# Kernel tuning notes

Measured on AMD Instinct MI355X. Metric: run time of the kernel, lower is better.

The kernel has to match this reference:

```python
import jax, jax.numpy as jnp
import numpy as np

N_SLOTS = 524288
DIM_MEM = 128
DIM_IN = 1024
SHIFT_RADIUS = 3
EPS = 1e-8  # torch cosine_similarity eps


def setup_inputs() -> dict:
    key = jax.random.key(0)
    k1, k2, k3, k4, k5 = jax.random.split(key, 5)
    n_factors = DIM_MEM + 1 + 1 + (2 * SHIFT_RADIUS + 1) + 1  # 138
    return {
        "input_from_controller": jax.random.normal(k1, (DIM_IN,), dtype=jnp.float32),
        "previous_weighting": jax.random.uniform(k2, (N_SLOTS,), dtype=jnp.float32),
        "memory": jax.random.normal(k3, (N_SLOTS, DIM_MEM), dtype=jnp.float32),
        "W_wf": jax.random.normal(k4, (DIM_IN, n_factors), dtype=jnp.float32) * 0.02,
        "b_wf": jax.random.normal(k5, (n_factors,), dtype=jnp.float32) * 0.02,
    }


def _get_weighting(input_from_controller, previous_weighting, memory, W_wf, b_wf):
    factors = input_from_controller @ W_wf + b_wf  # [138]
    M = DIM_MEM
    key_v = factors[:M]                       # [M]
    key_s = factors[M]                        # scalar (beta)
    gate = jax.nn.softmax(factors[M + 1:M + 2])      # size-1 softmax -> 1.0 (faithful)
    shift_w = jax.nn.softmax(factors[M + 2:M + 2 + 2 * SHIFT_RADIUS + 1])  # [2r+1]
    sharpening = jax.nn.relu(factors[-1]) + 1.0

    # content addressing: cosine similarity of each memory row with key_v
    mem_norm = jnp.maximum(jnp.linalg.norm(memory, axis=1), EPS)  # [N]
    key_norm = jnp.maximum(jnp.linalg.norm(key_v), EPS)
    content_w = (memory @ key_v) / (mem_norm * key_norm)          # [N]
    content_w = jax.nn.softmax(key_s * content_w)

    gated_w = content_w * gate[0] + (1.0 - gate[0]) * previous_weighting

    # circular convolution: shifted[i] = sum_j gated[(i - r + j) % N] * shift_w[j]
    shifted_w = jnp.zeros_like(gated_w)
    for j in range(2 * SHIFT_RADIUS + 1):  # small fixed tap count (7)
        shifted_w = shifted_w + shift_w[j] * jnp.roll(gated_w, SHIFT_RADIUS - j)

    pw = shifted_w ** sharpening
    return pw / pw.sum()


def reference(input_from_controller, previous_weighting, memory, W_wf, b_wf):
    w = _get_weighting(input_from_controller, previous_weighting, memory, W_wf, b_wf)
    read_vector = w @ memory  # read head forward
    return read_vector
```

## Files before the change

kernel.cpp:

```cpp
#include <hip/hip_runtime.h>
#include <math.h>

#define N_SLOTS 524288
#define DIM_MEM 128
#define DIM_IN 1024
#define NFACT 138
#define EPSF 1e-8f

#define RPB 256
#define CHUNK 64
#define NCH (RPB / CHUNK)
#define FB (N_SLOTS / RPB)

#define WS_NEED ((size_t)4096 + (size_t)(DIM_MEM + 1) * FB * 4)

__global__ __launch_bounds__(256) void k_factors(const float* __restrict__ x,
                                                 const float* __restrict__ W,
                                                 const float* __restrict__ b,
                                                 float* __restrict__ factors) {
    __shared__ float wred[4];
    const int j = blockIdx.x;
    const int t = threadIdx.x;
    float acc = 0.f;
    #pragma unroll
    for (int i = t; i < DIM_IN; i += 256)
        acc = fmaf(x[i], W[(size_t)i * NFACT + j], acc);
    #pragma unroll
    for (int off = 32; off; off >>= 1) acc += __shfl_xor(acc, off, 64);
    if ((t & 63) == 0) wred[t >> 6] = acc;
    __syncthreads();
    if (t == 0)
        factors[j] = wred[0] + wred[1] + wred[2] + wred[3] + b[j];
}

__global__ __launch_bounds__(256) void k_fused(const float* __restrict__ mem,
                                               const float* __restrict__ f,
                                               float* __restrict__ sc) {
    __shared__ float d_sh[12];
    __shared__ float e_sh[CHUNK + 8];
    __shared__ float w_sh[CHUNK];
    __shared__ float colpart[8][DIM_MEM];
    __shared__ float psum[8];

    const int tid  = threadIdx.x;
    const int lane = tid & 31;
    const int hw   = tid >> 5;

    if (tid < 64) {
        float fl = f[tid], fh = f[tid + 64];
        float v = fl * fl + fh * fh;
        #pragma unroll
        for (int off = 32; off; off >>= 1) v += __shfl_xor(v, off, 64);
        if (tid == 0) {
            float key_norm = fmaxf(sqrtf(v), EPSF);
            d_sh[0] = f[128] / key_norm;
            float m = f[130];
            #pragma unroll
            for (int q = 1; q < 7; ++q) m = fmaxf(m, f[130 + q]);
            float e[7], s = 0.f;
            #pragma unroll
            for (int q = 0; q < 7; ++q) { e[q] = __expf(f[130 + q] - m); s += e[q]; }
            #pragma unroll
            for (int q = 0; q < 7; ++q) d_sh[1 + q] = e[q] / s;
            d_sh[8] = fmaxf(f[137], 0.f) + 1.f;
        }
    }
    __syncthreads();

    const float4* __restrict__ mem4 = (const float4*)mem;
    const float4 k4 = ((const float4*)f)[lane];
    const float d0 = d_sh[0];
    const float sharp = d_sh[8];
    float sw[7];
    #pragma unroll
    for (int d = 0; d < 7; ++d) sw[d] = d_sh[1 + d];

    float4 acc = make_float4(0.f, 0.f, 0.f, 0.f);
    float wsum = 0.f;
    const int base = blockIdx.x * RPB;

    float4 row[2][8];
    #pragma unroll
    for (int j = 0; j < 8; ++j)
        row[0][j] = mem4[(size_t)(base + hw * 8 + j) * 32 + lane];

    #pragma unroll
    for (int c = 0; c < NCH; ++c) {
        const int cur = c & 1;
        const int nxt = cur ^ 1;
        const int r0 = base + c * CHUNK;

        #pragma unroll
        for (int j = 0; j < 8; ++j) {
            float4 m = row[cur][j];
            float dp = m.x * k4.x + m.y * k4.y + m.z * k4.z + m.w * k4.w;
            float np = m.x * m.x + m.y * m.y + m.z * m.z + m.w * m.w;
            #pragma unroll
            for (int off = 16; off; off >>= 1) {
                dp += __shfl_xor(dp, off, 32);
                np += __shfl_xor(np, off, 32);
            }
            if (lane == 0)
                e_sh[3 + hw * 8 + j] = __expf(d0 * dp / fmaxf(sqrtf(np), EPSF));
        }
        if (hw < 6) {
            int hr = (hw < 3) ? (r0 - 3 + hw) : (r0 + CHUNK + (hw - 3));
            hr &= (N_SLOTS - 1);
            const int p = (hw < 3) ? hw : (CHUNK + hw);
            float4 m = mem4[(size_t)hr * 32 + lane];
            float dp = m.x * k4.x + m.y * k4.y + m.z * k4.z + m.w * k4.w;
            float np = m.x * m.x + m.y * m.y + m.z * m.z + m.w * m.w;
            #pragma unroll
            for (int off = 16; off; off >>= 1) {
                dp += __shfl_xor(dp, off, 32);
                np += __shfl_xor(np, off, 32);
            }
            if (lane == 0)
                e_sh[p] = __expf(d0 * dp / fmaxf(sqrtf(np), EPSF));
        }
        if (c + 1 < NCH) {
            const int nb = r0 + CHUNK + hw * 8;
            #pragma unroll
            for (int j = 0; j < 8; ++j)
                row[nxt][j] = mem4[(size_t)(nb + j) * 32 + lane];
        }
        __syncthreads();

        if (tid < CHUNK) {
            float t = 0.f;
            #pragma unroll
            for (int d = 0; d < 7; ++d) t = fmaf(sw[d], e_sh[tid + d], t);
            w_sh[tid] = __expf(sharp * __logf(t));
        }
        __syncthreads();

        #pragma unroll
        for (int j = 0; j < 8; ++j) {
            float w = w_sh[hw * 8 + j];
            acc.x = fmaf(w, row[cur][j].x, acc.x);
            acc.y = fmaf(w, row[cur][j].y, acc.y);
            acc.z = fmaf(w, row[cur][j].z, acc.z);
            acc.w = fmaf(w, row[cur][j].w, acc.w);
            wsum += w;
        }
    }

    ((float4*)colpart[hw])[lane] = acc;
    if (lane == 0) psum[hw] = wsum;
    __syncthreads();
    if (tid < DIM_MEM) {
        float s = 0.f;
        #pragma unroll
        for (int h = 0; h < 8; ++h) s += colpart[h][tid];
        sc[(size_t)tid * FB + blockIdx.x] = s;
    }
    if (tid == 0) {
        float s = 0.f;
        #pragma unroll
        for (int h = 0; h < 8; ++h) s += psum[h];
        sc[(size_t)DIM_MEM * FB + blockIdx.x] = s;
    }
}

__global__ void k_reduce(const float* __restrict__ sc, float* __restrict__ out) {
    __shared__ float red[8];
    const int c = blockIdx.x;
    const int t = threadIdx.x;
    float s = 0.f, pv = 0.f;
    for (int b = t; b < FB; b += 256) {
        s  += sc[(size_t)c * FB + b];
        pv += sc[(size_t)DIM_MEM * FB + b];
    }
    #pragma unroll
    for (int off = 32; off; off >>= 1) {
        s  += __shfl_xor(s, off, 64);
        pv += __shfl_xor(pv, off, 64);
    }
    const int w = t >> 6;
    if ((t & 63) == 0) { red[w * 2] = s; red[w * 2 + 1] = pv; }
    __syncthreads();
    if (t == 0) {
        float S = 0.f, P = 0.f;
        #pragma unroll
        for (int i = 0; i < 4; ++i) { S += red[i * 2]; P += red[i * 2 + 1]; }
        out[c] = S / P;
    }
}

extern "C" void kernel_launch(void* const* d_in, const int* in_sizes, int n_in,
                              void* d_out, int out_size, void* d_ws, size_t ws_size,
                              hipStream_t stream) {
    (void)in_sizes; (void)n_in; (void)out_size; (void)ws_size;
    const float* x   = (const float*)d_in[0];
    const float* mem = (const float*)d_in[2];
    const float* W   = (const float*)d_in[3];
    const float* b   = (const float*)d_in[4];
    float* out = (float*)d_out;

    char*  ws      = (char*)d_ws;
    float* factors = (float*)ws;
    float* sc      = (float*)(ws + 4096);

    k_factors<<<NFACT, 256, 0, stream>>>(x, W, b, factors);
    k_fused<<<FB, 256, 0, stream>>>(mem, factors, sc);
    k_reduce<<<DIM_MEM, 256, 0, stream>>>(sc, out);
}
```

Measured before the change: 381.5 us.

## Map each memory row to 16 lanes with two float4 loads to cut shuffles

```diff
diff --git a/kernel.cpp b/kernel.cpp
--- a/kernel.cpp
+++ b/kernel.cpp
@@ -12,7 +12,13 @@
 #define NCH (RPB / CHUNK)
 #define FB (N_SLOTS / RPB)
 
-#define WS_NEED ((size_t)4096 + (size_t)(DIM_MEM + 1) * FB * 4)
+typedef float f4 __attribute__((ext_vector_type(4)));
+
+__device__ __forceinline__ float dot4(f4 a, f4 b) {
+    f4 t = a * b;
+    return (t.x + t.y) + (t.z + t.w);
+}
+
 
 __global__ __launch_bounds__(256) void k_factors(const float* __restrict__ x,
                                                  const float* __restrict__ W,
@@ -39,12 +45,14 @@
     __shared__ float d_sh[12];
     __shared__ float e_sh[CHUNK + 8];
     __shared__ float w_sh[CHUNK];
-    __shared__ float colpart[8][DIM_MEM];
-    __shared__ float psum[8];
-
-    const int tid  = threadIdx.x;
-    const int lane = tid & 31;
-    const int hw   = tid >> 5;
+    __shared__ float colpart[4][DIM_MEM] __attribute__((aligned(16)));
+    __shared__ float psum[4];
+
+    const int tid = threadIdx.x;
+    const int sub = tid & 15;
+    const int qw  = tid >> 4;
+    const int wv  = tid >> 6;
+    const int l6  = tid & 63;
 
     if (tid < 64) {
         float fl = f[tid], fh = f[tid + 64];
@@ -65,24 +73,31 @@
             d_sh[8] = fmaxf(f[137], 0.f) + 1.f;
         }
     }
-    __syncthreads();
-
-    const float4* __restrict__ mem4 = (const float4*)mem;
-    const float4 k4 = ((const float4*)f)[lane];
+
+    const f4* __restrict__ mem4 = (const f4*)mem;
+    const f4* __restrict__ kf4  = (const f4*)f;
+    const f4 ka = kf4[sub];
+    const f4 kb = kf4[16 + sub];
+
+    const int base = blockIdx.x * RPB;
+    f4 row[2][4][2];
+    #pragma unroll
+    for (int j = 0; j < 4; ++j) {
+        const size_t rr = (size_t)(base + qw * 4 + j) * 32;
+        row[0][j][0] = mem4[rr + sub];
+        row[0][j][1] = mem4[rr + 16 + sub];
+    }
+    __syncthreads();
+
     const float d0 = d_sh[0];
     const float sharp = d_sh[8];
     float sw[7];
     #pragma unroll
     for (int d = 0; d < 7; ++d) sw[d] = d_sh[1 + d];
 
-    float4 acc = make_float4(0.f, 0.f, 0.f, 0.f);
+    f4 acc0 = {0.f, 0.f, 0.f, 0.f};
+    f4 acc1 = {0.f, 0.f, 0.f, 0.f};
     float wsum = 0.f;
-    const int base = blockIdx.x * RPB;
-
-    float4 row[2][8];
-    #pragma unroll
-    for (int j = 0; j < 8; ++j)
-        row[0][j] = mem4[(size_t)(base + hw * 8 + j) * 32 + lane];
 
     #pragma unroll
     for (int c = 0; c < NCH; ++c) {
@@ -90,39 +105,47 @@
         const int nxt = cur ^ 1;
         const int r0 = base + c * CHUNK;
 
-        #pragma unroll
-        for (int j = 0; j < 8; ++j) {
-            float4 m = row[cur][j];
-            float dp = m.x * k4.x + m.y * k4.y + m.z * k4.z + m.w * k4.w;
-            float np = m.x * m.x + m.y * m.y + m.z * m.z + m.w * m.w;
-            #pragma unroll
-            for (int off = 16; off; off >>= 1) {
-                dp += __shfl_xor(dp, off, 32);
-                np += __shfl_xor(np, off, 32);
+        f4 ha = {0.f,0.f,0.f,0.f}, hb = {0.f,0.f,0.f,0.f};
+        int hp = 0;
+        if (qw < 6) {
+            int hr = (qw < 3) ? (r0 - 3 + qw) : (r0 + CHUNK + (qw - 3));
+            hr &= (N_SLOTS - 1);
+            hp = (qw < 3) ? qw : (CHUNK + qw);
+            ha = mem4[(size_t)hr * 32 + sub];
+            hb = mem4[(size_t)hr * 32 + 16 + sub];
+        }
+        if (c + 1 < NCH) {
+            #pragma unroll
+            for (int j = 0; j < 4; ++j) {
+                const size_t rr = (size_t)(r0 + CHUNK + qw * 4 + j) * 32;
+                row[nxt][j][0] = mem4[rr + sub];
+                row[nxt][j][1] = mem4[rr + 16 + sub];
             }
-            if (lane == 0)
-                e_sh[3 + hw * 8 + j] = __expf(d0 * dp / fmaxf(sqrtf(np), EPSF));
-        }
-        if (hw < 6) {
-            int hr = (hw < 3) ? (r0 - 3 + hw) : (r0 + CHUNK + (hw - 3));
-            hr &= (N_SLOTS - 1);
-            const int p = (hw < 3) ? hw : (CHUNK + hw);
-            float4 m = mem4[(size_t)hr * 32 + lane];
-            float dp = m.x * k4.x + m.y * k4.y + m.z * k4.z + m.w * k4.w;
-            float np = m.x * m.x + m.y * m.y + m.z * m.z + m.w * m.w;
-            #pragma unroll
-            for (int off = 16; off; off >>= 1) {
-                dp += __shfl_xor(dp, off, 32);
-                np += __shfl_xor(np, off, 32);
+        }
+
+        #pragma unroll
+        for (int j = 0; j < 4; ++j) {
+            float dp = dot4(row[cur][j][0], ka) + dot4(row[cur][j][1], kb);
+            float np = dot4(row[cur][j][0], row[cur][j][0])
+                     + dot4(row[cur][j][1], row[cur][j][1]);
+            #pragma unroll
+            for (int off = 1; off <= 8; off <<= 1) {
+                dp += __shfl_xor(dp, off, 64);
+                np += __shfl_xor(np, off, 64);
             }
-            if (lane == 0)
-                e_sh[p] = __expf(d0 * dp / fmaxf(sqrtf(np), EPSF));
-        }
-        if (c + 1 < NCH) {
-            const int nb = r0 + CHUNK + hw * 8;
-            #pragma unroll
-            for (int j = 0; j < 8; ++j)
-                row[nxt][j] = mem4[(size_t)(nb + j) * 32 + lane];
+            if (sub == 0)
+                e_sh[3 + qw * 4 + j] = __expf(d0 * dp / fmaxf(sqrtf(np), EPSF));
+        }
+        if (qw < 6) {
+            float dp = dot4(ha, ka) + dot4(hb, kb);
+            float np = dot4(ha, ha) + dot4(hb, hb);
+            #pragma unroll
+            for (int off = 1; off <= 8; off <<= 1) {
+                dp += __shfl_xor(dp, off, 64);
+                np += __shfl_xor(np, off, 64);
+            }
+            if (sub == 0)
+                e_sh[hp] = __expf(d0 * dp / fmaxf(sqrtf(np), EPSF));
         }
         __syncthreads();
 
@@ -135,31 +158,39 @@
         __syncthreads();
 
         #pragma unroll
-        for (int j = 0; j < 8; ++j) {
-            float w = w_sh[hw * 8 + j];
-            acc.x = fmaf(w, row[cur][j].x, acc.x);
-            acc.y = fmaf(w, row[cur][j].y, acc.y);
-            acc.z = fmaf(w, row[cur][j].z, acc.z);
-            acc.w = fmaf(w, row[cur][j].w, acc.w);
-            wsum += w;
-        }
-    }
-
-    ((float4*)colpart[hw])[lane] = acc;
-    if (lane == 0) psum[hw] = wsum;
+        for (int j = 0; j < 4; ++j) {
+            const float w = w_sh[qw * 4 + j];
+            acc0 += w * row[cur][j][0];
+            acc1 += w * row[cur][j][1];
+        }
+        if (sub == 0)
+            wsum += w_sh[qw * 4] + w_sh[qw * 4 + 1] + w_sh[qw * 4 + 2] + w_sh[qw * 4 + 3];
+    }
+
+    #pragma unroll
+    for (int off = 16; off <= 32; off <<= 1) {
+        acc0.x += __shfl_xor(acc0.x, off, 64);
+        acc0.y += __shfl_xor(acc0.y, off, 64);
+        acc0.z += __shfl_xor(acc0.z, off, 64);
+        acc0.w += __shfl_xor(acc0.w, off, 64);
+        acc1.x += __shfl_xor(acc1.x, off, 64);
+        acc1.y += __shfl_xor(acc1.y, off, 64);
+        acc1.z += __shfl_xor(acc1.z, off, 64);
+        acc1.w += __shfl_xor(acc1.w, off, 64);
+        wsum   += __shfl_xor(wsum,   off, 64);
+    }
+    if (l6 < 16) {
+        ((f4*)colpart[wv])[l6]      = acc0;
+        ((f4*)colpart[wv])[16 + l6] = acc1;
+    }
+    if (l6 == 0) psum[wv] = wsum;
     __syncthreads();
     if (tid < DIM_MEM) {
-        float s = 0.f;
-        #pragma unroll
-        for (int h = 0; h < 8; ++h) s += colpart[h][tid];
+        float s = colpart[0][tid] + colpart[1][tid] + colpart[2][tid] + colpart[3][tid];
         sc[(size_t)tid * FB + blockIdx.x] = s;
     }
-    if (tid == 0) {
-        float s = 0.f;
-        #pragma unroll
-        for (int h = 0; h < 8; ++h) s += psum[h];
-        sc[(size_t)DIM_MEM * FB + blockIdx.x] = s;
-    }
+    if (tid == 0)
+        sc[(size_t)DIM_MEM * FB + blockIdx.x] = psum[0] + psum[1] + psum[2] + psum[3];
 }
 
 __global__ void k_reduce(const float* __restrict__ sc, float* __restrict__ out) {
```

After: 376.4 us. About the same (-1.3%).
